# Kernel tuning notes

Measured on AMD Instinct MI355X. Metric: run time of the kernel, lower is better.

## Reference

```python
import jax, jax.numpy as jnp
import numpy as np

H_DIM = 1024
N_HEADS = 16
HEAD_D = H_DIM // N_HEADS  # 64


def setup_inputs() -> dict:
    key = jax.random.key(0)
    ks = jax.random.split(key, 10)
    B, T, C = 2, 2048, H_DIM
    init = 1.0 / np.sqrt(C)  # lecun_normal-scale stand-in
    src = jax.random.normal(ks[0], (B, T, C), dtype=jnp.float32)
    mask = jnp.ones((B, T), dtype=jnp.float32)  # unused when causal
    Wq = jax.random.normal(ks[1], (C, H_DIM), dtype=jnp.float32) * init
    Wk = jax.random.normal(ks[2], (C, H_DIM), dtype=jnp.float32) * init
    Wv = jax.random.normal(ks[3], (C, H_DIM), dtype=jnp.float32) * init
    Wo = jax.random.normal(ks[4], (H_DIM, H_DIM), dtype=jnp.float32) * init
    bq = jnp.zeros((H_DIM,), jnp.float32)
    bk = jnp.zeros((H_DIM,), jnp.float32)
    bv = jnp.zeros((H_DIM,), jnp.float32)
    bo = jnp.zeros((H_DIM,), jnp.float32)
    return {"src": src, "mask": mask, "Wq": Wq, "bq": bq, "Wk": Wk, "bk": bk,
            "Wv": Wv, "bv": bv, "Wo": Wo, "bo": bo}


def reference(src, mask, Wq, bq, Wk, bk, Wv, bv, Wo, bo):
    # MaskedCausalAttention forward, deterministic=True (dropout = identity),
    # use_causal_mask=True.
    B, T, C = src.shape
    N, D = N_HEADS, HEAD_D
    # q,k,v: [B, N, T, D]
    q = (src @ Wq + bq).reshape(B, T, N, D).transpose(0, 2, 1, 3)
    k = (src @ Wk + bk).reshape(B, T, N, D).transpose(0, 2, 1, 3)
    v = (src @ Wv + bv).reshape(B, T, N, D).transpose(0, 2, 1, 3)
    # scores: [B, N, T, T]
    scores = jnp.einsum('bntd,bnsd->bnts', q, k) / jnp.sqrt(jnp.float32(D))
    causal = jnp.tril(jnp.ones((T, T), dtype=bool))[None, None]
    scores = jnp.where(causal, scores, -jnp.inf)
    probs = jax.nn.softmax(scores, axis=-1)
    attn = jnp.einsum('bnts,bnsd->bntd', probs, v)  # [B, N, T, D]
    attn = attn.transpose(0, 2, 1, 3).reshape(B, T, N * D)
    return attn @ Wo + bo
```

## Files before the change

### kernel.cpp

```cpp
#include <hip/hip_runtime.h>
#include <hip/hip_bf16.h>

typedef __hip_bfloat16 bf16;
typedef __attribute__((ext_vector_type(8))) short short8;
typedef __attribute__((ext_vector_type(4))) float f32x4;

#define BATCH 2
#define SEQ   2048
#define HDIM  1024
#define NHEAD 16
#define DHEAD 64
#define MROWS (BATCH*SEQ)

#define QSCALE 0.18033688f

#define EXP2F(x) __builtin_amdgcn_exp2f(x)

static __device__ __forceinline__ short f2bs(float x) {
    __hip_bfloat16 h = (__hip_bfloat16)x;
    return *reinterpret_cast<short*>(&h);
}

static __device__ __forceinline__ void gload16(const void* g, void* l) {
    __builtin_amdgcn_global_load_lds(
        (const __attribute__((address_space(1))) unsigned int*)g,
        (__attribute__((address_space(3))) unsigned int*)l, 16, 0, 0);
}

__global__ __launch_bounds__(256) void cvt_f32_bf16(const float* __restrict__ x,
                                                    short* __restrict__ y) {
    int i = blockIdx.x * 256 + threadIdx.x;
    float4 v = ((const float4*)x)[i];
    ushort4 o;
    o.x = (unsigned short)f2bs(v.x);
    o.y = (unsigned short)f2bs(v.y);
    o.z = (unsigned short)f2bs(v.z);
    o.w = (unsigned short)f2bs(v.w);
    ((ushort4*)y)[i] = o;
}

__global__ __launch_bounds__(256) void transpose_w3(const float* __restrict__ W0,
        const float* __restrict__ W1, const float* __restrict__ W2,
        short* __restrict__ Wt) {
    const float* W = (blockIdx.z == 0) ? W0 : (blockIdx.z == 1) ? W1 : W2;
    const int row_off = blockIdx.z * 1024;
    __shared__ float t[64][65];
    const int k0 = blockIdx.y * 64, n0 = blockIdx.x * 64;
    const int tid = threadIdx.x;
#pragma unroll
    for (int i = 0; i < 16; i++) {
        int idx = tid + i * 256, r = idx >> 6, c = idx & 63;
        t[r][c] = W[(size_t)(k0 + r) * HDIM + n0 + c];
    }
    __syncthreads();
#pragma unroll
    for (int i = 0; i < 16; i++) {
        int idx = tid + i * 256, c = idx >> 6, r = idx & 63;
        Wt[(size_t)(row_off + n0 + c) * HDIM + k0 + r] = f2bs(t[r][c]);
    }
}

__global__ __launch_bounds__(256) void gemm_qkvo(const short* __restrict__ A,
        const short* __restrict__ Bt,
        const float* __restrict__ bq, const float* __restrict__ bk,
        const float* __restrict__ bv, const float* __restrict__ bo,
        short* __restrict__ Qout, short* __restrict__ Kout,
        short* __restrict__ Vtout, float* __restrict__ Oout,
        int region_override)
{
    __shared__ short As[8 * 512];
    __shared__ short Bs[8 * 512];
    const int tid = threadIdx.x, lane = tid & 63, w = tid >> 6;
    const int quad = lane >> 4, l15 = lane & 15;
    const int m0 = blockIdx.y * 128, n0 = blockIdx.x * 128;
    const int wr = w >> 1, wc = w & 1;

    const short* gsrc[4];
    short* ldst[4];
#pragma unroll
    for (int i = 0; i < 4; i++) {
        int u = w * 4 + i;
        if (u < 8) {
            gsrc[i] = A + (size_t)(m0 + u * 16 + l15) * HDIM + quad * 8;
            ldst[i] = &As[u * 512];
        } else {
            int c = u - 8;
            gsrc[i] = Bt + (size_t)(n0 + c * 16 + l15) * HDIM + quad * 8;
            ldst[i] = &Bs[c * 512];
        }
    }

    f32x4 acc[4][4];
#pragma unroll
    for (int i = 0; i < 4; i++)
#pragma unroll
        for (int j = 0; j < 4; j++) acc[i][j] = (f32x4){0.f, 0.f, 0.f, 0.f};

    for (int kk = 0; kk < HDIM / 32; ++kk) {
        __syncthreads();
#pragma unroll
        for (int i = 0; i < 4; i++) {
            gload16(gsrc[i], ldst[i]);
            gsrc[i] += 32;
        }
        __syncthreads();

        short8 af[4], bfr[4];
#pragma unroll
        for (int mi = 0; mi < 4; mi++)
            af[mi] = *(const short8*)&As[(wr * 4 + mi) * 512 + lane * 8];
#pragma unroll
        for (int ni = 0; ni < 4; ni++)
            bfr[ni] = *(const short8*)&Bs[(wc * 4 + ni) * 512 + lane * 8];
#pragma unroll
        for (int mi = 0; mi < 4; mi++)
#pragma unroll
            for (int ni = 0; ni < 4; ni++)
                acc[mi][ni] = __builtin_amdgcn_mfma_f32_16x16x32_bf16(
                                  af[mi], bfr[ni], acc[mi][ni], 0, 0, 0);
    }

    const int region = (region_override < 0) ? (n0 >> 10) : region_override;
    const float* bias = (region == 0) ? bq : (region == 1) ? bk
                       : (region == 2) ? bv : bo;
    const float oscale = (region == 0) ? QSCALE : 1.0f;

    float bvv[4];
    int nl4[4];
#pragma unroll
    for (int ni = 0; ni < 4; ni++) {
        int n = n0 + (wc * 4 + ni) * 16 + l15;
        nl4[ni] = n & 1023;
        bvv[ni] = bias[nl4[ni]];
    }

#pragma unroll
    for (int mi = 0; mi < 4; mi++) {
        int mB = m0 + (wr * 4 + mi) * 16 + quad * 4;
#pragma unroll
        for (int ni = 0; ni < 4; ni++) {
            int nl = nl4[ni];
            if (region == 2) {
                int bb = mB >> 11, t = mB & 2047;
                int h = nl >> 6, d = nl & 63;
                size_t base = ((size_t)((bb * NHEAD + h) * DHEAD + d)) * SEQ + t;
                ushort4 pk;
                pk.x = (unsigned short)f2bs(acc[mi][ni][0] + bvv[ni]);
                pk.y = (unsigned short)f2bs(acc[mi][ni][1] + bvv[ni]);
                pk.z = (unsigned short)f2bs(acc[mi][ni][2] + bvv[ni]);
                pk.w = (unsigned short)f2bs(acc[mi][ni][3] + bvv[ni]);
                *(ushort4*)(Vtout + base) = pk;
            } else if (region == 3) {
#pragma unroll
                for (int r = 0; r < 4; r++)
                    Oout[(size_t)(mB + r) * HDIM + nl] = acc[mi][ni][r] + bvv[ni];
            } else {
                short* C = (region == 0) ? Qout : Kout;
#pragma unroll
                for (int r = 0; r < 4; r++)
                    C[(size_t)(mB + r) * HDIM + nl] =
                        f2bs((acc[mi][ni][r] + bvv[ni]) * oscale);
            }
        }
    }
}

__global__ __launch_bounds__(256) void attn_mfma(const short* __restrict__ Qb,
        const short* __restrict__ Kb, const short* __restrict__ Vt,
        short* __restrict__ Ab)
{
    __shared__ short Ks[8 * 512];
    __shared__ short Vs[8 * 512];
    __shared__ short Ps[4 * 16 * 72];
    const int tid = threadIdx.x, lane = tid & 63, w = tid >> 6;
    const int quad = lane >> 4, l15 = lane & 15;
    const int b = blockIdx.z, head = blockIdx.y;

    const short* Kbh = Kb + (size_t)b * SEQ * HDIM + head * DHEAD;
    const short* Vth = Vt + (size_t)(b * NHEAD + head) * DHEAD * SEQ;
    short* Pw = &Ps[w * 1152];

    const int strips[2] = { (int)blockIdx.x, 31 - (int)blockIdx.x };

    for (int si = 0; si < 2; ++si) {
        const int strip = strips[si];
        const int qbase = strip * 64;
        const int qr = qbase + w * 16 + l15;

        const short* qptr = Qb + (size_t)(b * SEQ + qr) * HDIM + head * DHEAD + quad * 8;
        short8 bq0 = *(const short8*)qptr;
        short8 bq1 = *(const short8*)(qptr + 32);

        f32x4 o[4];
#pragma unroll
        for (int dt = 0; dt < 4; dt++) o[dt] = (f32x4){0.f, 0.f, 0.f, 0.f};
        float mrow = -3.0e38f, lrow = 0.f;

        for (int it = 0; it <= strip; ++it) {
            const int s0 = it * 64;
            __syncthreads();
#pragma unroll
            for (int i = 0; i < 4; i++) {
                int u = w * 4 + i;
                if (u < 8) {
                    int t = u >> 1, h = u & 1;
                    const short* g = Kbh + (size_t)(s0 + t * 16 + l15) * HDIM
                                     + h * 32 + quad * 8;
                    gload16(g, &Ks[u * 512]);
                } else {
                    int c = u - 8, dt = c >> 1, kh = c & 1;
                    const short* g = Vth + (size_t)(dt * 16 + l15) * SEQ
                                     + s0 + kh * 32 + quad * 8;
                    gload16(g, &Vs[c * 512]);
                }
            }
            __syncthreads();

            f32x4 sv[4];
#pragma unroll
            for (int t = 0; t < 4; t++) {
                sv[t] = (f32x4){0.f, 0.f, 0.f, 0.f};
                short8 k0 = *(const short8*)&Ks[(t * 2) * 512 + lane * 8];
                short8 k1 = *(const short8*)&Ks[(t * 2 + 1) * 512 + lane * 8];
                sv[t] = __builtin_amdgcn_mfma_f32_16x16x32_bf16(k0, bq0, sv[t], 0, 0, 0);
                sv[t] = __builtin_amdgcn_mfma_f32_16x16x32_bf16(k1, bq1, sv[t], 0, 0, 0);
            }

            float s[16];
#pragma unroll
            for (int t = 0; t < 4; t++)
#pragma unroll
                for (int r = 0; r < 4; r++) {
                    int key = s0 + t * 16 + quad * 4 + r;
                    s[t * 4 + r] = (key <= qr) ? sv[t][r] : -3.0e38f;
                }

            float tmx = s[0];
#pragma unroll
            for (int i = 1; i < 16; i++) tmx = fmaxf(tmx, s[i]);
            tmx = fmaxf(tmx, __shfl_xor(tmx, 16));
            tmx = fmaxf(tmx, __shfl_xor(tmx, 32));
            float mnew = fmaxf(mrow, tmx);
            float alpha = EXP2F(mrow - mnew);
            mrow = mnew;

            float ps = 0.f;
            short pb[16];
#pragma unroll
            for (int i = 0; i < 16; i++) {
                float p = EXP2F(s[i] - mnew);
                ps += p;
                pb[i] = f2bs(p);
            }
            ps += __shfl_xor(ps, 16);
            ps += __shfl_xor(ps, 32);
            lrow = lrow * alpha + ps;
#pragma unroll
            for (int dt = 0; dt < 4; dt++) o[dt] *= alpha;

#pragma unroll
            for (int t = 0; t < 4; t++) {
                ushort4 u4;
                u4.x = (unsigned short)pb[t * 4];
                u4.y = (unsigned short)pb[t * 4 + 1];
                u4.z = (unsigned short)pb[t * 4 + 2];
                u4.w = (unsigned short)pb[t * 4 + 3];
                *(ushort4*)&Pw[l15 * 72 + t * 16 + quad * 4] = u4;
            }
            short8 bp0 = *(const short8*)&Pw[l15 * 72 + quad * 8];
            short8 bp1 = *(const short8*)&Pw[l15 * 72 + 32 + quad * 8];

#pragma unroll
            for (int dt = 0; dt < 4; dt++) {
                short8 av0 = *(const short8*)&Vs[(dt * 2) * 512 + lane * 8];
                short8 av1 = *(const short8*)&Vs[(dt * 2 + 1) * 512 + lane * 8];
                o[dt] = __builtin_amdgcn_mfma_f32_16x16x32_bf16(av0, bp0, o[dt], 0, 0, 0);
                o[dt] = __builtin_amdgcn_mfma_f32_16x16x32_bf16(av1, bp1, o[dt], 0, 0, 0);
            }
        }

        const float inv = 1.f / lrow;
        const size_t obase = (size_t)(b * SEQ + qr) * HDIM + head * DHEAD;
#pragma unroll
        for (int dt = 0; dt < 4; dt++)
#pragma unroll
            for (int r = 0; r < 4; r++)
                Ab[obase + dt * 16 + quad * 4 + r] = f2bs(o[dt][r] * inv);
    }
}

extern "C" void kernel_launch(void* const* d_in, const int* in_sizes, int n_in,
                              void* d_out, int out_size, void* d_ws, size_t ws_size,
                              hipStream_t stream)
{
    const float* src = (const float*)d_in[0];
    const float* Wq = (const float*)d_in[2];
    const float* bq = (const float*)d_in[3];
    const float* Wk = (const float*)d_in[4];
    const float* bk = (const float*)d_in[5];
    const float* Wv = (const float*)d_in[6];
    const float* bv = (const float*)d_in[7];
    const float* Wo = (const float*)d_in[8];
    const float* bo = (const float*)d_in[9];
    float* out = (float*)d_out;

    short* Sb = (short*)d_ws;
    short* Qb = Sb + (size_t)MROWS * HDIM;
    short* Kb = Qb + (size_t)MROWS * HDIM;
    short* Vt = Kb + (size_t)MROWS * HDIM;
    short* Wt = Vt + (size_t)MROWS * HDIM;
    short* WtO = Sb;
    short* Ab = Qb;

    dim3 blk(256);
    const bool fused = (ws_size >= 39845888ull);

    cvt_f32_bf16<<<dim3(4096), blk, 0, stream>>>(src, Sb);

    if (fused) {
        transpose_w3<<<dim3(16, 16, 3), blk, 0, stream>>>(Wq, Wk, Wv, Wt);
        gemm_qkvo<<<dim3(24, 32), blk, 0, stream>>>(Sb, Wt, bq, bk, bv, bo,
                                                    Qb, Kb, Vt, nullptr, -1);
    } else {
        transpose_w3<<<dim3(16, 16, 1), blk, 0, stream>>>(Wq, Wq, Wq, Wt);
        gemm_qkvo<<<dim3(8, 32), blk, 0, stream>>>(Sb, Wt, bq, bk, bv, bo,
                                                   Qb, Kb, Vt, nullptr, 0);
        transpose_w3<<<dim3(16, 16, 1), blk, 0, stream>>>(Wk, Wk, Wk, Wt);
        gemm_qkvo<<<dim3(8, 32), blk, 0, stream>>>(Sb, Wt, bq, bk, bv, bo,
                                                   Qb, Kb, Vt, nullptr, 1);
        transpose_w3<<<dim3(16, 16, 1), blk, 0, stream>>>(Wv, Wv, Wv, Wt);
        gemm_qkvo<<<dim3(8, 32), blk, 0, stream>>>(Sb, Wt, bq, bk, bv, bo,
                                                   Qb, Kb, Vt, nullptr, 2);
    }

    attn_mfma<<<dim3(16, NHEAD, BATCH), blk, 0, stream>>>(Qb, Kb, Vt, Ab);

    transpose_w3<<<dim3(16, 16, 1), blk, 0, stream>>>(Wo, Wo, Wo, WtO);
    gemm_qkvo<<<dim3(8, 32), blk, 0, stream>>>(Ab, WtO, bq, bk, bv, bo,
                                               nullptr, nullptr, nullptr, out, 3);
}
```

Measured before the change: 239.6 us.

## Double-buffer GEMM and attention tiles, split GEMMs, fuse prep kernels

Merges the src conversion and Q/K/V weight transposes into one prep launch, and splits the generic GEMM into specialized QK, V and O kernels. V and O use 64-row tiles for more blocks. All GEMMs and the attention kernel now double-buffer LDS tiles so global loads overlap MFMA work, and the attention kernel skips causal masking on fully visible tiles. Workspace is re-planned to alias the QK weight buffer with the V output, removing the workspace-size fallback path at the cost of doubled LDS use.

Result: faster. 234.0 us (-2.3%).

```diff
diff --git a/kernel.cpp b/kernel.cpp
--- a/kernel.cpp
+++ b/kernel.cpp
@@ -13,7 +13,6 @@
 #define MROWS (BATCH*SEQ)
 
 #define QSCALE 0.18033688f
-
 #define EXP2F(x) __builtin_amdgcn_exp2f(x)
 
 static __device__ __forceinline__ short f2bs(float x) {
@@ -27,26 +26,32 @@
         (__attribute__((address_space(3))) unsigned int*)l, 16, 0, 0);
 }
 
-__global__ __launch_bounds__(256) void cvt_f32_bf16(const float* __restrict__ x,
-                                                    short* __restrict__ y) {
-    int i = blockIdx.x * 256 + threadIdx.x;
-    float4 v = ((const float4*)x)[i];
-    ushort4 o;
-    o.x = (unsigned short)f2bs(v.x);
-    o.y = (unsigned short)f2bs(v.y);
-    o.z = (unsigned short)f2bs(v.z);
-    o.w = (unsigned short)f2bs(v.w);
-    ((ushort4*)y)[i] = o;
-}
-
-__global__ __launch_bounds__(256) void transpose_w3(const float* __restrict__ W0,
-        const float* __restrict__ W1, const float* __restrict__ W2,
-        short* __restrict__ Wt) {
-    const float* W = (blockIdx.z == 0) ? W0 : (blockIdx.z == 1) ? W1 : W2;
-    const int row_off = blockIdx.z * 1024;
+__global__ __launch_bounds__(256) void prep1(const float* __restrict__ src,
+        const float* __restrict__ Wq, const float* __restrict__ Wk,
+        const float* __restrict__ Wv,
+        short* __restrict__ Sb, short* __restrict__ WqkT,
+        short* __restrict__ WvT)
+{
     __shared__ float t[64][65];
-    const int k0 = blockIdx.y * 64, n0 = blockIdx.x * 64;
-    const int tid = threadIdx.x;
+    const int bx = blockIdx.x, tid = threadIdx.x;
+    if (bx < 4096) {
+        int i = bx * 256 + tid;
+        float4 v = ((const float4*)src)[i];
+        ushort4 o;
+        o.x = (unsigned short)f2bs(v.x);
+        o.y = (unsigned short)f2bs(v.y);
+        o.z = (unsigned short)f2bs(v.z);
+        o.w = (unsigned short)f2bs(v.w);
+        ((ushort4*)Sb)[i] = o;
+        return;
+    }
+    const int tb = bx - 4096;
+    const int wsel = tb >> 8;
+    const float* W = (wsel == 0) ? Wq : (wsel == 1) ? Wk : Wv;
+    short* dst = (wsel < 2) ? WqkT : WvT;
+    const int roff = (wsel < 2) ? wsel * 1024 : 0;
+    const int t8 = tb & 255;
+    const int n0 = (t8 & 15) * 64, k0 = (t8 >> 4) * 64;
 #pragma unroll
     for (int i = 0; i < 16; i++) {
         int idx = tid + i * 256, r = idx >> 6, c = idx & 63;
@@ -56,37 +61,56 @@
 #pragma unroll
     for (int i = 0; i < 16; i++) {
         int idx = tid + i * 256, c = idx >> 6, r = idx & 63;
-        Wt[(size_t)(row_off + n0 + c) * HDIM + k0 + r] = f2bs(t[r][c]);
-    }
-}
-
-__global__ __launch_bounds__(256) void gemm_qkvo(const short* __restrict__ A,
+        dst[(size_t)(roff + n0 + c) * HDIM + k0 + r] = f2bs(t[r][c]);
+    }
+}
+
+__global__ __launch_bounds__(256) void transpose_one(const float* __restrict__ W,
+                                                     short* __restrict__ dst)
+{
+    __shared__ float t[64][65];
+    const int tid = threadIdx.x;
+    const int n0 = (blockIdx.x & 15) * 64, k0 = (blockIdx.x >> 4) * 64;
+#pragma unroll
+    for (int i = 0; i < 16; i++) {
+        int idx = tid + i * 256, r = idx >> 6, c = idx & 63;
+        t[r][c] = W[(size_t)(k0 + r) * HDIM + n0 + c];
+    }
+    __syncthreads();
+#pragma unroll
+    for (int i = 0; i < 16; i++) {
+        int idx = tid + i * 256, c = idx >> 6, r = idx & 63;
+        dst[(size_t)(n0 + c) * HDIM + k0 + r] = f2bs(t[r][c]);
+    }
+}
+
+__global__ __launch_bounds__(256) void gemm_qk(const short* __restrict__ A,
         const short* __restrict__ Bt,
         const float* __restrict__ bq, const float* __restrict__ bk,
-        const float* __restrict__ bv, const float* __restrict__ bo,
-        short* __restrict__ Qout, short* __restrict__ Kout,
-        short* __restrict__ Vtout, float* __restrict__ Oout,
-        int region_override)
-{
-    __shared__ short As[8 * 512];
-    __shared__ short Bs[8 * 512];
+        short* __restrict__ Qout, short* __restrict__ Kout)
+{
+    __shared__ short As[2][8 * 512];
+    __shared__ short Bs[2][8 * 512];
     const int tid = threadIdx.x, lane = tid & 63, w = tid >> 6;
     const int quad = lane >> 4, l15 = lane & 15;
     const int m0 = blockIdx.y * 128, n0 = blockIdx.x * 128;
     const int wr = w >> 1, wc = w & 1;
 
     const short* gsrc[4];
-    short* ldst[4];
+    short* dst0[4];
+    short* dst1[4];
 #pragma unroll
     for (int i = 0; i < 4; i++) {
         int u = w * 4 + i;
         if (u < 8) {
             gsrc[i] = A + (size_t)(m0 + u * 16 + l15) * HDIM + quad * 8;
-            ldst[i] = &As[u * 512];
+            dst0[i] = &As[0][u * 512];
+            dst1[i] = &As[1][u * 512];
         } else {
             int c = u - 8;
             gsrc[i] = Bt + (size_t)(n0 + c * 16 + l15) * HDIM + quad * 8;
-            ldst[i] = &Bs[c * 512];
+            dst0[i] = &Bs[0][c * 512];
+            dst1[i] = &Bs[1][c * 512];
         }
     }
 
@@ -96,71 +120,213 @@
 #pragma unroll
         for (int j = 0; j < 4; j++) acc[i][j] = (f32x4){0.f, 0.f, 0.f, 0.f};
 
-    for (int kk = 0; kk < HDIM / 32; ++kk) {
-        __syncthreads();
-#pragma unroll
-        for (int i = 0; i < 4; i++) {
-            gload16(gsrc[i], ldst[i]);
-            gsrc[i] += 32;
-        }
-        __syncthreads();
-
+#pragma unroll
+    for (int i = 0; i < 4; i++) { gload16(gsrc[i], dst0[i]); gsrc[i] += 32; }
+    __syncthreads();
+
+    for (int kk = 0; kk < 32; ++kk) {
+        const int cur = kk & 1;
+        if (kk < 31) {
+#pragma unroll
+            for (int i = 0; i < 4; i++) {
+                gload16(gsrc[i], cur ? dst0[i] : dst1[i]);
+                gsrc[i] += 32;
+            }
+        }
         short8 af[4], bfr[4];
 #pragma unroll
         for (int mi = 0; mi < 4; mi++)
-            af[mi] = *(const short8*)&As[(wr * 4 + mi) * 512 + lane * 8];
+            af[mi] = *(const short8*)&As[cur][(wr * 4 + mi) * 512 + lane * 8];
 #pragma unroll
         for (int ni = 0; ni < 4; ni++)
-            bfr[ni] = *(const short8*)&Bs[(wc * 4 + ni) * 512 + lane * 8];
+            bfr[ni] = *(const short8*)&Bs[cur][(wc * 4 + ni) * 512 + lane * 8];
 #pragma unroll
         for (int mi = 0; mi < 4; mi++)
 #pragma unroll
             for (int ni = 0; ni < 4; ni++)
                 acc[mi][ni] = __builtin_amdgcn_mfma_f32_16x16x32_bf16(
                                   af[mi], bfr[ni], acc[mi][ni], 0, 0, 0);
-    }
-
-    const int region = (region_override < 0) ? (n0 >> 10) : region_override;
-    const float* bias = (region == 0) ? bq : (region == 1) ? bk
-                       : (region == 2) ? bv : bo;
-    const float oscale = (region == 0) ? QSCALE : 1.0f;
-
-    float bvv[4];
-    int nl4[4];
-#pragma unroll
-    for (int ni = 0; ni < 4; ni++) {
-        int n = n0 + (wc * 4 + ni) * 16 + l15;
-        nl4[ni] = n & 1023;
-        bvv[ni] = bias[nl4[ni]];
-    }
+        __syncthreads();
+    }
+
+    const int region = n0 >> 10;
+    const float* bias = region ? bk : bq;
+    const float oscale = region ? 1.0f : QSCALE;
+    short* C = region ? Kout : Qout;
 
 #pragma unroll
     for (int mi = 0; mi < 4; mi++) {
         int mB = m0 + (wr * 4 + mi) * 16 + quad * 4;
 #pragma unroll
         for (int ni = 0; ni < 4; ni++) {
-            int nl = nl4[ni];
-            if (region == 2) {
-                int bb = mB >> 11, t = mB & 2047;
-                int h = nl >> 6, d = nl & 63;
-                size_t base = ((size_t)((bb * NHEAD + h) * DHEAD + d)) * SEQ + t;
-                ushort4 pk;
-                pk.x = (unsigned short)f2bs(acc[mi][ni][0] + bvv[ni]);
-                pk.y = (unsigned short)f2bs(acc[mi][ni][1] + bvv[ni]);
-                pk.z = (unsigned short)f2bs(acc[mi][ni][2] + bvv[ni]);
-                pk.w = (unsigned short)f2bs(acc[mi][ni][3] + bvv[ni]);
-                *(ushort4*)(Vtout + base) = pk;
-            } else if (region == 3) {
-#pragma unroll
-                for (int r = 0; r < 4; r++)
-                    Oout[(size_t)(mB + r) * HDIM + nl] = acc[mi][ni][r] + bvv[ni];
-            } else {
-                short* C = (region == 0) ? Qout : Kout;
-#pragma unroll
-                for (int r = 0; r < 4; r++)
-                    C[(size_t)(mB + r) * HDIM + nl] =
-                        f2bs((acc[mi][ni][r] + bvv[ni]) * oscale);
-            }
+            int nl = (n0 + (wc * 4 + ni) * 16 + l15) & 1023;
+            float bb = bias[nl];
+#pragma unroll
+            for (int r = 0; r < 4; r++)
+                C[(size_t)(mB + r) * HDIM + nl] =
+                    f2bs((acc[mi][ni][r] + bb) * oscale);
+        }
+    }
+}
+
+__global__ __launch_bounds__(256) void gemm_v(const short* __restrict__ A,
+        const short* __restrict__ Bt, const float* __restrict__ bv,
+        short* __restrict__ Vtout)
+{
+    __shared__ short As[2][4 * 512];
+    __shared__ short Bs[2][8 * 512];
+    const int tid = threadIdx.x, lane = tid & 63, w = tid >> 6;
+    const int quad = lane >> 4, l15 = lane & 15;
+    const int m0 = blockIdx.y * 64, n0 = blockIdx.x * 128;
+    const int wr = w >> 1, wc = w & 1;
+
+    const short* gsrc[3];
+    short* dst0[3];
+    short* dst1[3];
+#pragma unroll
+    for (int i = 0; i < 3; i++) {
+        int u = w * 3 + i;
+        if (u < 4) {
+            gsrc[i] = A + (size_t)(m0 + u * 16 + l15) * HDIM + quad * 8;
+            dst0[i] = &As[0][u * 512];
+            dst1[i] = &As[1][u * 512];
+        } else {
+            int c = u - 4;
+            gsrc[i] = Bt + (size_t)(n0 + c * 16 + l15) * HDIM + quad * 8;
+            dst0[i] = &Bs[0][c * 512];
+            dst1[i] = &Bs[1][c * 512];
+        }
+    }
+
+    f32x4 acc[2][4];
+#pragma unroll
+    for (int i = 0; i < 2; i++)
+#pragma unroll
+        for (int j = 0; j < 4; j++) acc[i][j] = (f32x4){0.f, 0.f, 0.f, 0.f};
+
+#pragma unroll
+    for (int i = 0; i < 3; i++) { gload16(gsrc[i], dst0[i]); gsrc[i] += 32; }
+    __syncthreads();
+
+    for (int kk = 0; kk < 32; ++kk) {
+        const int cur = kk & 1;
+        if (kk < 31) {
+#pragma unroll
+            for (int i = 0; i < 3; i++) {
+                gload16(gsrc[i], cur ? dst0[i] : dst1[i]);
+                gsrc[i] += 32;
+            }
+        }
+        short8 af[2], bfr[4];
+#pragma unroll
+        for (int mi = 0; mi < 2; mi++)
+            af[mi] = *(const short8*)&As[cur][(wr * 2 + mi) * 512 + lane * 8];
+#pragma unroll
+        for (int ni = 0; ni < 4; ni++)
+            bfr[ni] = *(const short8*)&Bs[cur][(wc * 4 + ni) * 512 + lane * 8];
+#pragma unroll
+        for (int mi = 0; mi < 2; mi++)
+#pragma unroll
+            for (int ni = 0; ni < 4; ni++)
+                acc[mi][ni] = __builtin_amdgcn_mfma_f32_16x16x32_bf16(
+                                  af[mi], bfr[ni], acc[mi][ni], 0, 0, 0);
+        __syncthreads();
+    }
+
+#pragma unroll
+    for (int mi = 0; mi < 2; mi++) {
+        int mB = m0 + (wr * 2 + mi) * 16 + quad * 4;
+        int bb = mB >> 11, t = mB & 2047;
+#pragma unroll
+        for (int ni = 0; ni < 4; ni++) {
+            int n = n0 + (wc * 4 + ni) * 16 + l15;
+            int h = n >> 6, d = n & 63;
+            float bvv = bv[n];
+            size_t base = ((size_t)((bb * NHEAD + h) * DHEAD + d)) * SEQ + t;
+            ushort4 pk;
+            pk.x = (unsigned short)f2bs(acc[mi][ni][0] + bvv);
+            pk.y = (unsigned short)f2bs(acc[mi][ni][1] + bvv);
+            pk.z = (unsigned short)f2bs(acc[mi][ni][2] + bvv);
+            pk.w = (unsigned short)f2bs(acc[mi][ni][3] + bvv);
+            *(ushort4*)(Vtout + base) = pk;
+        }
+    }
+}
+
+__global__ __launch_bounds__(256) void gemm_o(const short* __restrict__ A,
+        const short* __restrict__ Bt, const float* __restrict__ bo,
+        float* __restrict__ Out)
+{
+    __shared__ short As[2][4 * 512];
+    __shared__ short Bs[2][8 * 512];
+    const int tid = threadIdx.x, lane = tid & 63, w = tid >> 6;
+    const int quad = lane >> 4, l15 = lane & 15;
+    const int m0 = blockIdx.y * 64, n0 = blockIdx.x * 128;
+    const int wr = w >> 1, wc = w & 1;
+
+    const short* gsrc[3];
+    short* dst0[3];
+    short* dst1[3];
+#pragma unroll
+    for (int i = 0; i < 3; i++) {
+        int u = w * 3 + i;
+        if (u < 4) {
+            gsrc[i] = A + (size_t)(m0 + u * 16 + l15) * HDIM + quad * 8;
+            dst0[i] = &As[0][u * 512];
+            dst1[i] = &As[1][u * 512];
+        } else {
+            int c = u - 4;
+            gsrc[i] = Bt + (size_t)(n0 + c * 16 + l15) * HDIM + quad * 8;
+            dst0[i] = &Bs[0][c * 512];
+            dst1[i] = &Bs[1][c * 512];
+        }
+    }
+
+    f32x4 acc[2][4];
+#pragma unroll
+    for (int i = 0; i < 2; i++)
+#pragma unroll
+        for (int j = 0; j < 4; j++) acc[i][j] = (f32x4){0.f, 0.f, 0.f, 0.f};
+
+#pragma unroll
+    for (int i = 0; i < 3; i++) { gload16(gsrc[i], dst0[i]); gsrc[i] += 32; }
+    __syncthreads();
+
+    for (int kk = 0; kk < 32; ++kk) {
+        const int cur = kk & 1;
+        if (kk < 31) {
+#pragma unroll
+            for (int i = 0; i < 3; i++) {
+                gload16(gsrc[i], cur ? dst0[i] : dst1[i]);
+                gsrc[i] += 32;
+            }
+        }
+        short8 af[2], bfr[4];
+#pragma unroll
+        for (int mi = 0; mi < 2; mi++)
+            af[mi] = *(const short8*)&As[cur][(wr * 2 + mi) * 512 + lane * 8];
+#pragma unroll
+        for (int ni = 0; ni < 4; ni++)
+            bfr[ni] = *(const short8*)&Bs[cur][(wc * 4 + ni) * 512 + lane * 8];
+#pragma unroll
+        for (int mi = 0; mi < 2; mi++)
+#pragma unroll
+            for (int ni = 0; ni < 4; ni++)
+                acc[mi][ni] = __builtin_amdgcn_mfma_f32_16x16x32_bf16(
+                                  af[mi], bfr[ni], acc[mi][ni], 0, 0, 0);
+        __syncthreads();
+    }
+
+#pragma unroll
+    for (int mi = 0; mi < 2; mi++) {
+        int mB = m0 + (wr * 2 + mi) * 16 + quad * 4;
+#pragma unroll
+        for (int ni = 0; ni < 4; ni++) {
+            int n = n0 + (wc * 4 + ni) * 16 + l15;
+            float bb = bo[n];
+#pragma unroll
+            for (int r = 0; r < 4; r++)
+                Out[(size_t)(mB + r) * HDIM + n] = acc[mi][ni][r] + bb;
         }
     }
 }
@@ -169,8 +335,8 @@
         const short* __restrict__ Kb, const short* __restrict__ Vt,
         short* __restrict__ Ab)
 {
-    __shared__ short Ks[8 * 512];
-    __shared__ short Vs[8 * 512];
+    __shared__ short Ks[2][8 * 512];
+    __shared__ short Vs[2][8 * 512];
     __shared__ short Ps[4 * 16 * 72];
     const int tid = threadIdx.x, lane = tid & 63, w = tid >> 6;
     const int quad = lane >> 4, l15 = lane & 15;
@@ -180,12 +346,31 @@
     const short* Vth = Vt + (size_t)(b * NHEAD + head) * DHEAD * SEQ;
     short* Pw = &Ps[w * 1152];
 
+    auto stage = [&](int s0, int bf) {
+#pragma unroll
+        for (int i = 0; i < 4; i++) {
+            int u = w * 4 + i;
+            if (u < 8) {
+                int t = u >> 1, h = u & 1;
+                const short* g = Kbh + (size_t)(s0 + t * 16 + l15) * HDIM
+                                 + h * 32 + quad * 8;
+                gload16(g, &Ks[bf][u * 512]);
+            } else {
+                int c = u - 8, dt = c >> 1, kh = c & 1;
+                const short* g = Vth + (size_t)(dt * 16 + l15) * SEQ
+                                 + s0 + kh * 32 + quad * 8;
+                gload16(g, &Vs[bf][c * 512]);
+            }
+        }
+    };
+
     const int strips[2] = { (int)blockIdx.x, 31 - (int)blockIdx.x };
 
     for (int si = 0; si < 2; ++si) {
         const int strip = strips[si];
         const int qbase = strip * 64;
         const int qr = qbase + w * 16 + l15;
+        const int qwave = qbase + w * 16;
 
         const short* qptr = Qb + (size_t)(b * SEQ + qr) * HDIM + head * DHEAD + quad * 8;
         short8 bq0 = *(const short8*)qptr;
@@ -196,44 +381,39 @@
         for (int dt = 0; dt < 4; dt++) o[dt] = (f32x4){0.f, 0.f, 0.f, 0.f};
         float mrow = -3.0e38f, lrow = 0.f;
 
+        stage(0, 0);
+        __syncthreads();
+
         for (int it = 0; it <= strip; ++it) {
             const int s0 = it * 64;
-            __syncthreads();
-#pragma unroll
-            for (int i = 0; i < 4; i++) {
-                int u = w * 4 + i;
-                if (u < 8) {
-                    int t = u >> 1, h = u & 1;
-                    const short* g = Kbh + (size_t)(s0 + t * 16 + l15) * HDIM
-                                     + h * 32 + quad * 8;
-                    gload16(g, &Ks[u * 512]);
-                } else {
-                    int c = u - 8, dt = c >> 1, kh = c & 1;
-                    const short* g = Vth + (size_t)(dt * 16 + l15) * SEQ
-                                     + s0 + kh * 32 + quad * 8;
-                    gload16(g, &Vs[c * 512]);
-                }
-            }
-            __syncthreads();
+            const int cur = it & 1;
+            if (it < strip) stage(s0 + 64, cur ^ 1);
 
             f32x4 sv[4];
 #pragma unroll
             for (int t = 0; t < 4; t++) {
                 sv[t] = (f32x4){0.f, 0.f, 0.f, 0.f};
-                short8 k0 = *(const short8*)&Ks[(t * 2) * 512 + lane * 8];
-                short8 k1 = *(const short8*)&Ks[(t * 2 + 1) * 512 + lane * 8];
+                short8 k0 = *(const short8*)&Ks[cur][(t * 2) * 512 + lane * 8];
+                short8 k1 = *(const short8*)&Ks[cur][(t * 2 + 1) * 512 + lane * 8];
                 sv[t] = __builtin_amdgcn_mfma_f32_16x16x32_bf16(k0, bq0, sv[t], 0, 0, 0);
                 sv[t] = __builtin_amdgcn_mfma_f32_16x16x32_bf16(k1, bq1, sv[t], 0, 0, 0);
             }
 
             float s[16];
-#pragma unroll
-            for (int t = 0; t < 4; t++)
-#pragma unroll
-                for (int r = 0; r < 4; r++) {
-                    int key = s0 + t * 16 + quad * 4 + r;
-                    s[t * 4 + r] = (key <= qr) ? sv[t][r] : -3.0e38f;
-                }
+            if (s0 + 63 <= qwave) {
+#pragma unroll
+                for (int t = 0; t < 4; t++)
+#pragma unroll
+                    for (int r = 0; r < 4; r++) s[t * 4 + r] = sv[t][r];
+            } else {
+#pragma unroll
+                for (int t = 0; t < 4; t++)
+#pragma unroll
+                    for (int r = 0; r < 4; r++) {
+                        int key = s0 + t * 16 + quad * 4 + r;
+                        s[t * 4 + r] = (key <= qr) ? sv[t][r] : -3.0e38f;
+                    }
+            }
 
             float tmx = s[0];
 #pragma unroll
@@ -272,11 +452,12 @@
 
 #pragma unroll
             for (int dt = 0; dt < 4; dt++) {
-                short8 av0 = *(const short8*)&Vs[(dt * 2) * 512 + lane * 8];
-                short8 av1 = *(const short8*)&Vs[(dt * 2 + 1) * 512 + lane * 8];
+                short8 av0 = *(const short8*)&Vs[cur][(dt * 2) * 512 + lane * 8];
+                short8 av1 = *(const short8*)&Vs[cur][(dt * 2 + 1) * 512 + lane * 8];
                 o[dt] = __builtin_amdgcn_mfma_f32_16x16x32_bf16(av0, bp0, o[dt], 0, 0, 0);
                 o[dt] = __builtin_amdgcn_mfma_f32_16x16x32_bf16(av1, bp1, o[dt], 0, 0, 0);
             }
+            __syncthreads();
         }
 
         const float inv = 1.f / lrow;
@@ -304,38 +485,25 @@
     const float* bo = (const float*)d_in[9];
     float* out = (float*)d_out;
 
-    short* Sb = (short*)d_ws;
-    short* Qb = Sb + (size_t)MROWS * HDIM;
-    short* Kb = Qb + (size_t)MROWS * HDIM;
-    short* Vt = Kb + (size_t)MROWS * HDIM;
-    short* Wt = Vt + (size_t)MROWS * HDIM;
-    short* WtO = Sb;
-    short* Ab = Qb;
+    short* Sb   = (short*)d_ws;
+    short* Qb   = Sb + (size_t)MROWS * HDIM;
+    short* Kb   = Qb + (size_t)MROWS * HDIM;
+    short* Vt   = Kb + (size_t)MROWS * HDIM;
+    short* slot = Vt + (size_t)MROWS * HDIM;
+    short* WqkT = Vt;
+    short* Ab   = Qb;
 
     dim3 blk(256);
-    const bool fused = (ws_size >= 39845888ull);
-
-    cvt_f32_bf16<<<dim3(4096), blk, 0, stream>>>(src, Sb);
-
-    if (fused) {
-        transpose_w3<<<dim3(16, 16, 3), blk, 0, stream>>>(Wq, Wk, Wv, Wt);
-        gemm_qkvo<<<dim3(24, 32), blk, 0, stream>>>(Sb, Wt, bq, bk, bv, bo,
-                                                    Qb, Kb, Vt, nullptr, -1);
-    } else {
-        transpose_w3<<<dim3(16, 16, 1), blk, 0, stream>>>(Wq, Wq, Wq, Wt);
-        gemm_qkvo<<<dim3(8, 32), blk, 0, stream>>>(Sb, Wt, bq, bk, bv, bo,
-                                                   Qb, Kb, Vt, nullptr, 0);
-        transpose_w3<<<dim3(16, 16, 1), blk, 0, stream>>>(Wk, Wk, Wk, Wt);
-        gemm_qkvo<<<dim3(8, 32), blk, 0, stream>>>(Sb, Wt, bq, bk, bv, bo,
-                                                   Qb, Kb, Vt, nullptr, 1);
-        transpose_w3<<<dim3(16, 16, 1), blk, 0, stream>>>(Wv, Wv, Wv, Wt);
-        gemm_qkvo<<<dim3(8, 32), blk, 0, stream>>>(Sb, Wt, bq, bk, bv, bo,
-                                                   Qb, Kb, Vt, nullptr, 2);
-    }
+
+    prep1<<<dim3(4096 + 768), blk, 0, stream>>>(src, Wq, Wk, Wv, Sb, WqkT, slot);
+
+    gemm_qk<<<dim3(16, 32), blk, 0, stream>>>(Sb, WqkT, bq, bk, Qb, Kb);
+
+    gemm_v<<<dim3(8, 64), blk, 0, stream>>>(Sb, slot, bv, Vt);
+
+    transpose_one<<<dim3(256), blk, 0, stream>>>(Wo, slot);
 
     attn_mfma<<<dim3(16, NHEAD, BATCH), blk, 0, stream>>>(Qb, Kb, Vt, Ab);
 
-    transpose_w3<<<dim3(16, 16, 1), blk, 0, stream>>>(Wo, Wo, Wo, WtO);
-    gemm_qkvo<<<dim3(8, 32), blk, 0, stream>>>(Ab, WtO, bq, bk, bv, bo,
-                                               nullptr, nullptr, nullptr, out, 3);
-}
+    gemm_o<<<dim3(8, 64), blk, 0, stream>>>(Ab, slot, bo, out);
+}
```
